# Kernel tuning notes

Hardware: AMD Instinct MI355X
Metric: run time of the kernel (lower is better)

Reference implementation:

```python
import jax, jax.numpy as jnp
import numpy as np

EMBED_DIM = 4096
NUM_HEADS = 32
HEAD_DIM = EMBED_DIM // NUM_HEADS  # 128
KV_LEN = 8192


def setup_inputs() -> dict:
    key = jax.random.key(0)
    ks = jax.random.split(key, 12)
    s = 1.0 / np.sqrt(EMBED_DIM)
    return {
        "x": jax.random.normal(ks[0], (EMBED_DIM,), jnp.float32),
        "v": jax.random.normal(ks[1], (KV_LEN, NUM_HEADS, HEAD_DIM), jnp.float32),
        "k": jax.random.normal(ks[2], (KV_LEN, NUM_HEADS, HEAD_DIM), jnp.float32),
        "Wv": jax.random.normal(ks[3], (EMBED_DIM, EMBED_DIM), jnp.float32) * s,
        "bv": jnp.zeros((EMBED_DIM,), jnp.float32),
        "Wq": jax.random.normal(ks[4], (EMBED_DIM, EMBED_DIM), jnp.float32) * s,
        "bq": jnp.zeros((EMBED_DIM,), jnp.float32),
        "Wk": jax.random.normal(ks[5], (EMBED_DIM, EMBED_DIM), jnp.float32) * s,
        "bk": jnp.zeros((EMBED_DIM,), jnp.float32),
        "Wo": jax.random.normal(ks[6], (EMBED_DIM, EMBED_DIM), jnp.float32) * s,
        "bo": jnp.zeros((EMBED_DIM,), jnp.float32),
    }


def reference(x, v, k, Wv, bv, Wq, bq, Wk, bk, Wo, bo):
    # Project the single incoming token to q/k/v heads.
    v_i = (x @ Wv + bv).reshape(1, NUM_HEADS, HEAD_DIM)
    q_i = (x @ Wq + bq).reshape(NUM_HEADS, HEAD_DIM)
    k_i = (x @ Wk + bk).reshape(1, NUM_HEADS, HEAD_DIM)
    # Rolling cache: drop oldest slot, append new token.
    v = jnp.concatenate((v[1:], v_i), axis=0)  # [KV_LEN, H, D]
    k = jnp.concatenate((k[1:], k_i), axis=0)
    # Valid slots are those with any nonzero value entry.
    mask = jnp.any(v != 0, axis=(1, 2))  # [KV_LEN]
    attn = jnp.einsum('hd,khd->hk', q_i, k) / jnp.sqrt(jnp.float32(HEAD_DIM))
    attn = jnp.where(mask, attn, -jnp.inf)
    attn = jax.nn.softmax(attn, axis=-1)  # [H, KV_LEN]
    values = jnp.einsum('hk,khd->hd', attn, v).reshape(EMBED_DIM)
    out_i = values @ Wo + bo
    return (out_i, v, k)
```

## Files before the change

### kernel.cpp

```cpp
#include <hip/hip_runtime.h>

#define E 4096
#define H 32
#define L 8192
#define SCALE 0.08838834764831845f

#define WS_PART  0
#define WS_QFIN  393216
#define WS_KFIN  397312
#define WS_VFIN  401408
#define WS_NUMP  405504
#define WS_DENP  471040
#define WS_OPART 472064

typedef float fv4 __attribute__((ext_vector_type(4)));

__device__ __forceinline__ fv4 ntload4(const float* p) {
  return __builtin_nontemporal_load(reinterpret_cast<const fv4*>(p));
}
__device__ __forceinline__ void ntstore4(float* p, fv4 v) {
  __builtin_nontemporal_store(v, reinterpret_cast<fv4*>(p));
}

__global__ __launch_bounds__(256) void zero_np(float* __restrict__ ws) {
  int i = blockIdx.x * 256 + threadIdx.x;
  if (i < (WS_OPART - WS_NUMP)) ws[WS_NUMP + i] = 0.f;
}

__global__ __launch_bounds__(256) void gemv_qkv(const float* __restrict__ x,
    const float* __restrict__ Wq, const float* __restrict__ Wk,
    const float* __restrict__ Wv, float* __restrict__ ws) {
  int b = blockIdx.x;
  int mat = b >> 7;
  int rem = b & 127;
  int chunk = rem >> 2;
  int g = rem & 3;
  const float* W = (mat == 0) ? Wq : (mat == 1) ? Wk : Wv;
  int t = threadIdx.x;
  int j = (g << 10) + (t << 2);
  float ax = 0.f, ay = 0.f, az = 0.f, aw = 0.f;
  int i0 = chunk << 7;
  #pragma unroll 8
  for (int r = 0; r < 128; ++r) {
    int i = i0 + r;
    float xi = x[i];
    const fv4 w4 = ntload4(W + (size_t)i * E + j);
    ax += xi * w4.x; ay += xi * w4.y; az += xi * w4.z; aw += xi * w4.w;
  }
  fv4 val = {ax, ay, az, aw};
  ntstore4(ws + WS_PART + (mat << 17) + (chunk << 12) + j, val);
}

__global__ __launch_bounds__(256) void qkvred(const float* __restrict__ bq,
    const float* __restrict__ bk, const float* __restrict__ bv,
    float* __restrict__ ws) {
  int e = blockIdx.x * 256 + threadIdx.x;
  int mat = e >> 12;
  int col = e & 4095;
  const float* part = ws + WS_PART + (mat << 17);
  float s = 0.f;
  #pragma unroll 8
  for (int c = 0; c < 32; ++c) s += part[(c << 12) + col];
  const float* bias = (mat == 0) ? bq : (mat == 1) ? bk : bv;
  ws[WS_QFIN + (mat << 12) + col] = s + bias[col];
}

#define SLOTS 16
__device__ __forceinline__ void load_slot(int o, int t,
    const float* __restrict__ kin, const float* __restrict__ vin,
    const float* __restrict__ ws, fv4 k4[4], fv4 v4[4]) {
  if (o < L - 1) {
    const float* ks = kin + (size_t)(o + 1) * E;
    const float* vs = vin + (size_t)(o + 1) * E;
    #pragma unroll
    for (int c = 0; c < 4; ++c) {
      int e = (c << 10) + (t << 2);
      k4[c] = ntload4(ks + e);
      v4[c] = ntload4(vs + e);
    }
  } else {
    #pragma unroll
    for (int c = 0; c < 4; ++c) {
      int e = (c << 10) + (t << 2);
      k4[c] = *reinterpret_cast<const fv4*>(ws + WS_KFIN + e);
      v4[c] = *reinterpret_cast<const fv4*>(ws + WS_VFIN + e);
    }
  }
}

__global__ __launch_bounds__(256) void kvpass(const float* __restrict__ kin,
    const float* __restrict__ vin,
    float* __restrict__ kout, float* __restrict__ vout,
    float* __restrict__ ws) {
  __shared__ float wlds[SLOTS * 32];
  __shared__ int flags[SLOTS];
  int t = threadIdx.x;
  if (t < SLOTS) flags[t] = 0;
  fv4 q4[4];
  #pragma unroll
  for (int c = 0; c < 4; ++c)
    q4[c] = *reinterpret_cast<const fv4*>(ws + WS_QFIN + (c << 10) + (t << 2));
  __syncthreads();

  float accx[4] = {0,0,0,0}, accy[4] = {0,0,0,0};
  float accz[4] = {0,0,0,0}, accw[4] = {0,0,0,0};
  int base = blockIdx.x * SLOTS;
  int rep = blockIdx.x & 15;

  fv4 kc[4], vc[4], kn[4], vn[4];
  load_slot(base, t, kin, vin, ws, kc, vc);

  for (int s = 0; s < SLOTS; ++s) {
    int o = base + s;
    if (s + 1 < SLOTS)
      load_slot(o + 1, t, kin, vin, ws, kn, vn);
    float* kd = kout + (size_t)o * E;
    float* vd = vout + (size_t)o * E;
    #pragma unroll
    for (int c = 0; c < 4; ++c) {
      int e = (c << 10) + (t << 2);
      ntstore4(kd + e, kc[c]);
      ntstore4(vd + e, vc[c]);
    }
    bool nz = false;
    #pragma unroll
    for (int c = 0; c < 4; ++c) {
      float pp = kc[c].x * q4[c].x + kc[c].y * q4[c].y +
                 kc[c].z * q4[c].z + kc[c].w * q4[c].w;
      #pragma unroll
      for (int off = 16; off >= 1; off >>= 1)
        pp += __shfl_xor(pp, off);
      float w = __expf(pp * SCALE);
      accx[c] += w * vc[c].x; accy[c] += w * vc[c].y;
      accz[c] += w * vc[c].z; accw[c] += w * vc[c].w;
      if ((t & 31) == 0) wlds[(s << 5) + (c << 3) + (t >> 5)] = w;
      nz = nz || vc[c].x != 0.f || vc[c].y != 0.f || vc[c].z != 0.f || vc[c].w != 0.f;
    }
    unsigned long long b = __ballot(nz);
    if ((t & 63) == 0 && b != 0ULL) atomicOr(&flags[s], 1);
    #pragma unroll
    for (int c = 0; c < 4; ++c) { kc[c] = kn[c]; vc[c] = vn[c]; }
  }
  float* num = ws + WS_NUMP + (rep << 12);
  #pragma unroll
  for (int c = 0; c < 4; ++c) {
    int e = (c << 10) + (t << 2);
    atomicAdd(num + e + 0, accx[c]);
    atomicAdd(num + e + 1, accy[c]);
    atomicAdd(num + e + 2, accz[c]);
    atomicAdd(num + e + 3, accw[c]);
  }
  __syncthreads();
  if (t < 32) {
    float d = 0.f;
    #pragma unroll
    for (int s = 0; s < SLOTS; ++s)
      if (flags[s]) d += wlds[(s << 5) + t];
    atomicAdd(ws + WS_DENP + (rep << 6) + t, d);
  }
}

__global__ __launch_bounds__(256) void gemv_out(const float* __restrict__ Wo,
    const float* __restrict__ bo, float* __restrict__ ws) {
  int b = blockIdx.x;
  int chunk = b >> 2;
  int g = b & 3;
  int t = threadIdx.x;
  int j = (g << 10) + (t << 2);
  __shared__ float vals[64];
  int i0 = chunk << 6;
  if (t < 64) {
    float s = 0.f;
    #pragma unroll
    for (int r = 0; r < 16; ++r) s += ws[WS_NUMP + (r << 12) + i0 + t];
    float d = 0.f;
    int h = chunk >> 1;
    #pragma unroll
    for (int r = 0; r < 16; ++r) d += ws[WS_DENP + (r << 6) + h];
    vals[t] = s / d;
  }
  __syncthreads();
  float ax = 0.f, ay = 0.f, az = 0.f, aw = 0.f;
  #pragma unroll 4
  for (int r = 0; r < 64; ++r) {
    int i = i0 + r;
    float vi = vals[r];
    const fv4 w4 = ntload4(Wo + (size_t)i * E + j);
    ax += vi * w4.x; ay += vi * w4.y; az += vi * w4.z; aw += vi * w4.w;
  }
  if (chunk == 0) {
    const fv4 b4 = *reinterpret_cast<const fv4*>(bo + j);
    ax += b4.x; ay += b4.y; az += b4.z; aw += b4.w;
  }
  fv4 val = {ax, ay, az, aw};
  ntstore4(ws + WS_OPART + (chunk << 12) + j, val);
}

__global__ __launch_bounds__(256) void writeout(const float* __restrict__ ws,
                                                float* __restrict__ out) {
  int i = blockIdx.x * 256 + threadIdx.x;
  float s = 0.f;
  #pragma unroll 8
  for (int c = 0; c < 64; ++c) s += ws[WS_OPART + (c << 12) + i];
  out[i] = s;
}

extern "C" void kernel_launch(void* const* d_in, const int* in_sizes, int n_in,
                              void* d_out, int out_size, void* d_ws, size_t ws_size,
                              hipStream_t stream) {
  const float* x   = (const float*)d_in[0];
  const float* vin = (const float*)d_in[1];
  const float* kin = (const float*)d_in[2];
  const float* Wv  = (const float*)d_in[3];
  const float* bv  = (const float*)d_in[4];
  const float* Wq  = (const float*)d_in[5];
  const float* bq  = (const float*)d_in[6];
  const float* Wk  = (const float*)d_in[7];
  const float* bk  = (const float*)d_in[8];
  const float* Wo  = (const float*)d_in[9];
  const float* bo  = (const float*)d_in[10];
  float* out  = (float*)d_out;
  float* vout = out + E;
  float* kout = vout + (size_t)L * E;
  float* ws   = (float*)d_ws;

  zero_np<<<(WS_OPART - WS_NUMP + 255) / 256, 256, 0, stream>>>(ws);
  gemv_qkv<<<384, 256, 0, stream>>>(x, Wq, Wk, Wv, ws);
  qkvred<<<48, 256, 0, stream>>>(bq, bk, bv, ws);
  kvpass<<<L / SLOTS, 256, 0, stream>>>(kin, vin, kout, vout, ws);
  gemv_out<<<256, 256, 0, stream>>>(Wo, bo, ws);
  writeout<<<16, 256, 0, stream>>>(ws, out);
}
```

Before: 174.6 us.

## Split cache shift into device memcpys and keep attention kernel read-only

The fused attention pass no longer writes the rolled K/V caches. Instead, two device-to-device memcpys copy the shifted cache rows, and a small kernel writes the new last slot. The attention kernel also switches K/V loads from nontemporal to regular loads. This removes stores from the attention loop but makes K and V be read a second time from HBM by the copies, which run serially on the same stream.

```diff
diff --git a/kernel.cpp b/kernel.cpp
--- a/kernel.cpp
+++ b/kernel.cpp
@@ -75,8 +75,8 @@
     #pragma unroll
     for (int c = 0; c < 4; ++c) {
       int e = (c << 10) + (t << 2);
-      k4[c] = ntload4(ks + e);
-      v4[c] = ntload4(vs + e);
+      k4[c] = *reinterpret_cast<const fv4*>(ks + e);
+      v4[c] = *reinterpret_cast<const fv4*>(vs + e);
     }
   } else {
     #pragma unroll
@@ -88,10 +88,8 @@
   }
 }
 
-__global__ __launch_bounds__(256) void kvpass(const float* __restrict__ kin,
-    const float* __restrict__ vin,
-    float* __restrict__ kout, float* __restrict__ vout,
-    float* __restrict__ ws) {
+__global__ __launch_bounds__(256) void attn(const float* __restrict__ kin,
+    const float* __restrict__ vin, float* __restrict__ ws) {
   __shared__ float wlds[SLOTS * 32];
   __shared__ int flags[SLOTS];
   int t = threadIdx.x;
@@ -114,14 +112,6 @@
     int o = base + s;
     if (s + 1 < SLOTS)
       load_slot(o + 1, t, kin, vin, ws, kn, vn);
-    float* kd = kout + (size_t)o * E;
-    float* vd = vout + (size_t)o * E;
-    #pragma unroll
-    for (int c = 0; c < 4; ++c) {
-      int e = (c << 10) + (t << 2);
-      ntstore4(kd + e, kc[c]);
-      ntstore4(vd + e, vc[c]);
-    }
     bool nz = false;
     #pragma unroll
     for (int c = 0; c < 4; ++c) {
@@ -157,6 +147,18 @@
     for (int s = 0; s < SLOTS; ++s)
       if (flags[s]) d += wlds[(s << 5) + t];
     atomicAdd(ws + WS_DENP + (rep << 6) + t, d);
+  }
+}
+
+__global__ __launch_bounds__(256) void lastslot(const float* __restrict__ ws,
+    float* __restrict__ kout, float* __restrict__ vout) {
+  int idx = (blockIdx.x * 256 + threadIdx.x) << 2;
+  if (idx < E) {
+    fv4 k = *reinterpret_cast<const fv4*>(ws + WS_KFIN + idx);
+    ntstore4(kout + (size_t)(L - 1) * E + idx, k);
+  } else {
+    fv4 v = *reinterpret_cast<const fv4*>(ws + WS_VFIN + idx - E);
+    ntstore4(vout + (size_t)(L - 1) * E + idx - E, v);
   }
 }
 
@@ -227,7 +229,12 @@
   zero_np<<<(WS_OPART - WS_NUMP + 255) / 256, 256, 0, stream>>>(ws);
   gemv_qkv<<<384, 256, 0, stream>>>(x, Wq, Wk, Wv, ws);
   qkvred<<<48, 256, 0, stream>>>(bq, bk, bv, ws);
-  kvpass<<<L / SLOTS, 256, 0, stream>>>(kin, vin, kout, vout, ws);
+  attn<<<L / SLOTS, 256, 0, stream>>>(kin, vin, ws);
+  hipMemcpyAsync(vout, vin + E, (size_t)(L - 1) * E * sizeof(float),
+                 hipMemcpyDeviceToDevice, stream);
+  hipMemcpyAsync(kout, kin + E, (size_t)(L - 1) * E * sizeof(float),
+                 hipMemcpyDeviceToDevice, stream);
+  lastslot<<<8, 256, 0, stream>>>(ws, kout, vout);
   gemv_out<<<256, 256, 0, stream>>>(Wo, bo, ws);
   writeout<<<16, 256, 0, stream>>>(ws, out);
 }
```

After: 258.9 us. +48.3%, slower.
